# Kernel optimization log

Measured on AMD Instinct MI355X. Metric: run time of the kernel, lower is better.

The kernel has to match this reference:

```python
import jax, jax.numpy as jnp
import numpy as np

N = 50000
E = 800000
IN_C, HID_C, OUT_C = 5, 64, 32


def setup_inputs() -> dict:
    key = jax.random.key(0)
    ks = jax.random.split(key, 9)
    x = jax.random.normal(ks[0], (N, IN_C), dtype=jnp.float32)
    edge_index = jax.random.randint(ks[1], (2, E), 0, N, dtype=jnp.int64)
    # SAGEConv params: lin_l (neighbor path, has bias), lin_r (root path, no bias)
    def lin(k, fan_out, fan_in):
        s = 1.0 / np.sqrt(fan_in)
        return jax.random.uniform(k, (fan_out, fan_in), jnp.float32, -s, s)
    W1l = lin(ks[2], HID_C, IN_C); b1 = jnp.zeros((HID_C,), jnp.float32); W1r = lin(ks[3], HID_C, IN_C)
    W2l = lin(ks[4], HID_C, HID_C); b2 = jnp.zeros((HID_C,), jnp.float32); W2r = lin(ks[5], HID_C, HID_C)
    W3l = lin(ks[6], OUT_C, HID_C); b3 = jnp.zeros((OUT_C,), jnp.float32); W3r = lin(ks[7], OUT_C, HID_C)
    return {"x": x, "edge_index": edge_index,
            "W1l": W1l, "b1": b1, "W1r": W1r,
            "W2l": W2l, "b2": b2, "W2r": W2r,
            "W3l": W3l, "b3": b3, "W3r": W3r}


def _sage_conv(x, src, dst, inv_deg, Wl, bl, Wr):
    # PyG SAGEConv (aggr='mean'): out = lin_l(mean_j x_j) + lin_r(x)
    msg = x[src]                                          # [E, d_in] gather
    agg = jax.ops.segment_sum(msg, dst, num_segments=N)   # [N, d_in] scatter-add
    mean = agg * inv_deg                                  # mean aggregation
    return mean @ Wl.T + bl + x @ Wr.T


def reference(x, edge_index, W1l, b1, W1r, W2l, b2, W2r, W3l, b3, W3r):
    src, dst = edge_index[0], edge_index[1]
    deg = jax.ops.segment_sum(jnp.ones((E,), x.dtype), dst, num_segments=N)
    inv_deg = (1.0 / jnp.maximum(deg, 1.0))[:, None]      # [N, 1]
    h = jax.nn.relu(_sage_conv(x, src, dst, inv_deg, W1l, b1, W1r))
    # F.dropout(p=0.2, training=self.training): identity in eval mode
    h = jax.nn.relu(_sage_conv(h, src, dst, inv_deg, W2l, b2, W2r))
    out = _sage_conv(h, src, dst, inv_deg, W3l, b3, W3r)
    return out
```

## Files before the change

### kernel.cpp

```cpp
#include <hip/hip_runtime.h>
#include <hip/hip_fp16.h>


#define N_NODES 50000
#define N_EDGES 800000
#define IN_C 5
#define HID_C 64
#define OUT_C 32

#define NB 196
#define BCAP 6144
#define BWG 256
#define BCH (N_EDGES / BWG)

typedef __attribute__((ext_vector_type(8))) short bf16x8;
typedef __attribute__((ext_vector_type(4))) float f32x4;

__device__ __forceinline__ int rfl(int v) { return __builtin_amdgcn_readfirstlane(v); }
__device__ __forceinline__ float lanebc(float v, int l) {
    return __int_as_float(__builtin_amdgcn_readlane(__float_as_int(v), l));
}
__device__ __forceinline__ unsigned short f2bf(float f) {
    unsigned u = __float_as_uint(f);
    return (unsigned short)((u + 0x7fffu + ((u >> 16) & 1u)) >> 16);
}
__device__ __forceinline__ float bf2f(unsigned short b) {
    return __uint_as_float(((unsigned)b) << 16);
}
__device__ __forceinline__ float2 unpk_h2(unsigned u) {
    __half2 h = *(__half2*)&u;
    return __half22float2(h);
}


__global__ __launch_bounds__(256) void k_prep(
    const float* __restrict__ W2l, const float* __restrict__ W2r,
    const float* __restrict__ W3l, const float* __restrict__ W3r,
    unsigned short* __restrict__ W2hi, unsigned short* __restrict__ W2lo,
    unsigned short* __restrict__ W3hi, unsigned short* __restrict__ W3lo,
    int* __restrict__ gcur) {
    if (blockIdx.x == 0 && threadIdx.x < NB) gcur[threadIdx.x] = 0;
    const int t = blockIdx.x * 256 + threadIdx.x;
    const int stride = gridDim.x * 256;
    for (int p = t; p < 64 * 128; p += stride) {
        int j = p >> 7, k = p & 127;
        float w = (k < 64) ? W2l[j * 64 + k] : W2r[j * 64 + (k - 64)];
        unsigned short h = f2bf(w);
        W2hi[p] = h;
        W2lo[p] = f2bf(w - bf2f(h));
    }
    for (int p = t; p < 32 * 128; p += stride) {
        int j = p >> 7, k = p & 127;
        float w = (k < 64) ? W3l[j * 64 + k] : W3r[j * 64 + (k - 64)];
        unsigned short h = f2bf(w);
        W3hi[p] = h;
        W3lo[p] = f2bf(w - bf2f(h));
    }
}


__global__ __launch_bounds__(256) void k_bucket(const int* __restrict__ ei,
                                                int* __restrict__ gcur,
                                                unsigned* __restrict__ ebuf) {
    __shared__ int hist[NB];
    __shared__ int loff[NB];
    __shared__ int cur[NB];
    __shared__ int gbase[NB];
    __shared__ int scanb[256];
    __shared__ unsigned stage[BCH];
    const int t = threadIdx.x;
    const int c0 = blockIdx.x * BCH;

    if (t < NB) hist[t] = 0;
    __syncthreads();
    for (int i = t; i < BCH; i += 256) {
        int d = ei[N_EDGES + c0 + i];
        atomicAdd(&hist[d >> 8], 1);
    }
    __syncthreads();
    scanb[t] = (t < NB) ? hist[t] : 0;
    __syncthreads();
#pragma unroll
    for (int o = 1; o < 256; o <<= 1) {
        int v = scanb[t];
        int a = (t >= o) ? scanb[t - o] : 0;
        __syncthreads();
        scanb[t] = v + a;
        __syncthreads();
    }
    if (t < NB) {
        int ex = (t == 0) ? 0 : scanb[t - 1];
        loff[t] = ex;
        cur[t] = ex;
        gbase[t] = atomicAdd(&gcur[t], hist[t]);
    }
    __syncthreads();
    for (int i = t; i < BCH; i += 256) {
        int d = ei[N_EDGES + c0 + i];
        int s = ei[c0 + i];
        int b = d >> 8;
        int p = atomicAdd(&cur[b], 1);
        stage[p] = ((unsigned)d << 16) | (unsigned)s;
    }
    __syncthreads();
    for (int i = t; i < BCH; i += 256) {
        unsigned ev = stage[i];
        int b = ev >> 24;
        int pos = gbase[b] + (i - loff[b]);
        if (pos < BCAP) ebuf[b * BCAP + pos] = ev;
    }
}

__global__ __launch_bounds__(256) void k_bsort(const int* __restrict__ gcur,
                                               const unsigned* __restrict__ ebuf,
                                               int* __restrict__ row_off,
                                               float* __restrict__ inv_deg,
                                               int* __restrict__ srcs) {
    __shared__ int sc[256];
    __shared__ int cnt[256];
    __shared__ int loff[256];
    __shared__ int cur[256];
    __shared__ int stage[BCAP];
    const int t = threadIdx.x;
    const int b = blockIdx.x;

    sc[t] = (t < NB) ? gcur[t] : 0;
    __syncthreads();
#pragma unroll
    for (int o = 1; o < 256; o <<= 1) {
        int v = sc[t];
        int a = (t >= o) ? sc[t - o] : 0;
        __syncthreads();
        sc[t] = v + a;
        __syncthreads();
    }
    const int base = (b == 0) ? 0 : sc[b - 1];
    const int nraw = gcur[b];
    const int n = nraw < BCAP ? nraw : BCAP;
    const int node0 = b << 8;
    const unsigned* eb = ebuf + b * BCAP;

    cnt[t] = 0;
    __syncthreads();
    for (int i = t; i < n; i += 256) atomicAdd(&cnt[(eb[i] >> 16) & 255], 1);
    __syncthreads();
    loff[t] = cnt[t];
    __syncthreads();
#pragma unroll
    for (int o = 1; o < 256; o <<= 1) {
        int v = loff[t];
        int a = (t >= o) ? loff[t - o] : 0;
        __syncthreads();
        loff[t] = v + a;
        __syncthreads();
    }
    int ex = loff[t] - cnt[t];
    cur[t] = ex;
    int node = node0 + t;
    if (node < N_NODES) {
        row_off[node] = base + ex;
        int d = cnt[t];
        inv_deg[node] = 1.0f / (float)(d > 1 ? d : 1);
    }
    if (b == 0 && t == 0) row_off[N_NODES] = N_EDGES;
    __syncthreads();
    for (int i = t; i < n; i += 256) {
        unsigned ev = eb[i];
        int p = atomicAdd(&cur[(ev >> 16) & 255], 1);
        stage[p] = (int)(ev & 0xFFFFu);
    }
    __syncthreads();
    for (int i = t; i < n; i += 256) srcs[base + i] = stage[i];
}


__global__ __launch_bounds__(256) void k_layer1(
    const float* __restrict__ x, const int* __restrict__ row_off,
    const int* __restrict__ srcs, const float* __restrict__ inv_deg,
    const float* __restrict__ W1l, const float* __restrict__ b1,
    const float* __restrict__ W1r, __half* __restrict__ h1) {
    const int t = threadIdx.x;
    const int lane = t & 63;
    const int v = blockIdx.x * 4 + (t >> 6);
    if (v >= N_NODES) return;
    const int sub = lane >> 3;
    const int c = lane & 7;

    float wl[IN_C], wr[IN_C];
#pragma unroll
    for (int i = 0; i < IN_C; ++i) {
        wl[i] = W1l[lane * IN_C + i];
        wr[i] = W1r[lane * IN_C + i];
    }
    float bb = b1[lane];

    int beg = rfl(row_off[v]);
    int end = rfl(row_off[v + 1]);
    float sum = 0.f;
    for (int e = beg; e < end; e += 8) {
        int o = e + sub;
        if (o < end && c < IN_C) sum += x[srcs[o] * IN_C + c];
    }
    sum += __shfl_xor(sum, 8, 64);
    sum += __shfl_xor(sum, 16, 64);
    sum += __shfl_xor(sum, 32, 64);
    float summ = sum * inv_deg[v];
    float xv = (lane < IN_C) ? x[v * IN_C + lane] : 0.f;
    float acc = bb;
#pragma unroll
    for (int i = 0; i < IN_C; ++i) {
        acc += wl[i] * lanebc(summ, i);
        acc += wr[i] * lanebc(xv, i);
    }
    h1[v * HID_C + lane] = __float2half(fmaxf(acc, 0.f));
}


template <typename T> __device__ __forceinline__ T cvt_out(float v);
template <> __device__ __forceinline__ float cvt_out<float>(float v) { return v; }
template <> __device__ __forceinline__ __half cvt_out<__half>(float v) { return __float2half(v); }

template <int DOUT, bool RELU, typename OutT>
__global__ __launch_bounds__(256) void k_fused(
    const __half* __restrict__ h, const int* __restrict__ row_off,
    const int* __restrict__ srcs, const float* __restrict__ inv_deg,
    const unsigned short* __restrict__ Whi, const unsigned short* __restrict__ Wlo,
    const float* __restrict__ bias, OutT* __restrict__ out) {
    constexpr int AP = 152;
    __shared__ __align__(16) unsigned short Ah[32][AP];
    __shared__ __align__(16) unsigned short Al[32][AP];
    const int t = threadIdx.x;
    const int lane = t & 63;
    const int w = t >> 6;
    const int ns = lane >> 3;
    const int cg = lane & 7;
    const int node0 = blockIdx.x * 32;
    const int m = w * 8 + ns;
    const int v = node0 + m;
    const bool valid = v < N_NODES;
    const uint4* h4 = (const uint4*)h;

    int beg = 0, deg = 0;
    if (valid) {
        beg = row_off[v];
        deg = row_off[v + 1] - beg;
    }

    float s0 = 0.f, s1 = 0.f, s2 = 0.f, s3 = 0.f;
    float s4 = 0.f, s5 = 0.f, s6 = 0.f, s7 = 0.f;
    for (int k = 0; k < deg; k += 4) {
        int i0 = srcs[beg + k];
        int i1 = (k + 1 < deg) ? srcs[beg + k + 1] : i0;
        int i2 = (k + 2 < deg) ? srcs[beg + k + 2] : i0;
        int i3 = (k + 3 < deg) ? srcs[beg + k + 3] : i0;
        uint4 u0 = h4[i0 * 8 + cg];
        uint4 u1 = h4[i1 * 8 + cg];
        uint4 u2 = h4[i2 * 8 + cg];
        uint4 u3 = h4[i3 * 8 + cg];
        {
            float2 a = unpk_h2(u0.x), b = unpk_h2(u0.y);
            float2 c = unpk_h2(u0.z), d = unpk_h2(u0.w);
            s0 += a.x; s1 += a.y; s2 += b.x; s3 += b.y;
            s4 += c.x; s5 += c.y; s6 += d.x; s7 += d.y;
        }
        if (k + 1 < deg) {
            float2 a = unpk_h2(u1.x), b = unpk_h2(u1.y);
            float2 c = unpk_h2(u1.z), d = unpk_h2(u1.w);
            s0 += a.x; s1 += a.y; s2 += b.x; s3 += b.y;
            s4 += c.x; s5 += c.y; s6 += d.x; s7 += d.y;
        }
        if (k + 2 < deg) {
            float2 a = unpk_h2(u2.x), b = unpk_h2(u2.y);
            float2 c = unpk_h2(u2.z), d = unpk_h2(u2.w);
            s0 += a.x; s1 += a.y; s2 += b.x; s3 += b.y;
            s4 += c.x; s5 += c.y; s6 += d.x; s7 += d.y;
        }
        if (k + 3 < deg) {
            float2 a = unpk_h2(u3.x), b = unpk_h2(u3.y);
            float2 c = unpk_h2(u3.z), d = unpk_h2(u3.w);
            s0 += a.x; s1 += a.y; s2 += b.x; s3 += b.y;
            s4 += c.x; s5 += c.y; s6 += d.x; s7 += d.y;
        }
    }

    uint4 ur = make_uint4(0u, 0u, 0u, 0u);
    float idg = 0.f;
    if (valid) {
        ur = h4[v * 8 + cg];
        idg = inv_deg[v];
    }
    float m0 = s0 * idg, m1 = s1 * idg, m2 = s2 * idg, m3 = s3 * idg;
    float m4 = s4 * idg, m5 = s5 * idg, m6 = s6 * idg, m7 = s7 * idg;

    {
        unsigned short a0 = f2bf(m0), a1 = f2bf(m1), a2 = f2bf(m2), a3 = f2bf(m3);
        unsigned short a4 = f2bf(m4), a5 = f2bf(m5), a6 = f2bf(m6), a7 = f2bf(m7);
        uint4 hi, lo;
        hi.x = (unsigned)a0 | ((unsigned)a1 << 16);
        hi.y = (unsigned)a2 | ((unsigned)a3 << 16);
        hi.z = (unsigned)a4 | ((unsigned)a5 << 16);
        hi.w = (unsigned)a6 | ((unsigned)a7 << 16);
        lo.x = (unsigned)f2bf(m0 - bf2f(a0)) | ((unsigned)f2bf(m1 - bf2f(a1)) << 16);
        lo.y = (unsigned)f2bf(m2 - bf2f(a2)) | ((unsigned)f2bf(m3 - bf2f(a3)) << 16);
        lo.z = (unsigned)f2bf(m4 - bf2f(a4)) | ((unsigned)f2bf(m5 - bf2f(a5)) << 16);
        lo.w = (unsigned)f2bf(m6 - bf2f(a6)) | ((unsigned)f2bf(m7 - bf2f(a7)) << 16);
        *(uint4*)&Ah[m][cg * 8] = hi;
        *(uint4*)&Al[m][cg * 8] = lo;
    }
    {
        float2 p0 = unpk_h2(ur.x), p1 = unpk_h2(ur.y);
        float2 p2 = unpk_h2(ur.z), p3 = unpk_h2(ur.w);
        unsigned short a0 = f2bf(p0.x), a1 = f2bf(p0.y), a2 = f2bf(p1.x), a3 = f2bf(p1.y);
        unsigned short a4 = f2bf(p2.x), a5 = f2bf(p2.y), a6 = f2bf(p3.x), a7 = f2bf(p3.y);
        uint4 hi, lo;
        hi.x = (unsigned)a0 | ((unsigned)a1 << 16);
        hi.y = (unsigned)a2 | ((unsigned)a3 << 16);
        hi.z = (unsigned)a4 | ((unsigned)a5 << 16);
        hi.w = (unsigned)a6 | ((unsigned)a7 << 16);
        lo.x = (unsigned)f2bf(p0.x - bf2f(a0)) | ((unsigned)f2bf(p0.y - bf2f(a1)) << 16);
        lo.y = (unsigned)f2bf(p1.x - bf2f(a2)) | ((unsigned)f2bf(p1.y - bf2f(a3)) << 16);
        lo.z = (unsigned)f2bf(p2.x - bf2f(a4)) | ((unsigned)f2bf(p2.y - bf2f(a5)) << 16);
        lo.w = (unsigned)f2bf(p3.x - bf2f(a6)) | ((unsigned)f2bf(p3.y - bf2f(a7)) << 16);
        *(uint4*)&Ah[m][64 + cg * 8] = hi;
        *(uint4*)&Al[m][64 + cg * 8] = lo;
    }
    __syncthreads();

    constexpr int CT = DOUT / 16;
    constexpr int NTILES = 2 * CT;
    const int r = lane & 15;
    const int quad = lane >> 4;
#pragma unroll
    for (int ti = w; ti < NTILES; ti += 4) {
        const int n = ti % CT;
        const int rh = ti / CT;
        f32x4 acc = (f32x4){0.f, 0.f, 0.f, 0.f};
#pragma unroll
        for (int ks = 0; ks < 4; ++ks) {
            bf16x8 ah = *(const bf16x8*)&Ah[rh * 16 + r][ks * 32 + quad * 8];
            bf16x8 al = *(const bf16x8*)&Al[rh * 16 + r][ks * 32 + quad * 8];
            const size_t wb = ((size_t)(n * 16 + r)) * 128 + ks * 32 + quad * 8;
            bf16x8 bh = *(const bf16x8*)(Whi + wb);
            bf16x8 bl = *(const bf16x8*)(Wlo + wb);
            acc = __builtin_amdgcn_mfma_f32_16x16x32_bf16(ah, bh, acc, 0, 0, 0);
            acc = __builtin_amdgcn_mfma_f32_16x16x32_bf16(ah, bl, acc, 0, 0, 0);
            acc = __builtin_amdgcn_mfma_f32_16x16x32_bf16(al, bh, acc, 0, 0, 0);
        }
        float bv = bias[n * 16 + r];
#pragma unroll
        for (int g = 0; g < 4; ++g) {
            int node = node0 + rh * 16 + quad * 4 + g;
            if (node < N_NODES) {
                float vv = acc[g] + bv;
                if (RELU) vv = fmaxf(vv, 0.f);
                out[(size_t)node * DOUT + n * 16 + r] = cvt_out<OutT>(vv);
            }
        }
    }
}


extern "C" void kernel_launch(void* const* d_in, const int* in_sizes, int n_in,
                              void* d_out, int out_size, void* d_ws, size_t ws_size,
                              hipStream_t stream) {
    const float* x   = (const float*)d_in[0];
    const int*   ei  = (const int*)d_in[1];
    const float* W1l = (const float*)d_in[2];
    const float* b1  = (const float*)d_in[3];
    const float* W1r = (const float*)d_in[4];
    const float* W2l = (const float*)d_in[5];
    const float* b2  = (const float*)d_in[6];
    const float* W2r = (const float*)d_in[7];
    const float* W3l = (const float*)d_in[8];
    const float* b3  = (const float*)d_in[9];
    const float* W3r = (const float*)d_in[10];

    char* ws = (char*)d_ws;
    size_t off = 0;
    auto alloc = [&](size_t bytes) -> char* {
        char* p = ws + off;
        off += (bytes + 255) & ~(size_t)255;
        return p;
    };
    int*      gcur   = (int*)alloc(NB * sizeof(int));
    int*      rowoff = (int*)alloc((N_NODES + 1) * sizeof(int));
    float*    invdeg = (float*)alloc(N_NODES * sizeof(float));
    int*      srcs   = (int*)alloc(N_EDGES * sizeof(int));
    unsigned* ebuf   = (unsigned*)alloc((size_t)NB * BCAP * sizeof(unsigned));
    __half*   h1     = (__half*)alloc((size_t)N_NODES * HID_C * sizeof(__half));
    __half*   h2     = (__half*)alloc((size_t)N_NODES * HID_C * sizeof(__half));
    unsigned short* W2hi = (unsigned short*)alloc(64 * 128 * 2);
    unsigned short* W2lo = (unsigned short*)alloc(64 * 128 * 2);
    unsigned short* W3hi = (unsigned short*)alloc(32 * 128 * 2);
    unsigned short* W3lo = (unsigned short*)alloc(32 * 128 * 2);

    k_prep<<<dim3(48), dim3(256), 0, stream>>>(W2l, W2r, W3l, W3r,
                                               W2hi, W2lo, W3hi, W3lo, gcur);
    k_bucket<<<dim3(BWG), dim3(256), 0, stream>>>(ei, gcur, ebuf);
    k_bsort<<<dim3(NB), dim3(256), 0, stream>>>(gcur, ebuf, rowoff, invdeg, srcs);

    k_layer1<<<dim3(N_NODES / 4), dim3(256), 0, stream>>>(
        x, rowoff, srcs, invdeg, W1l, b1, W1r, h1);

    const int FT = (N_NODES + 31) / 32;
    k_fused<HID_C, true, __half><<<dim3(FT), dim3(256), 0, stream>>>(
        h1, rowoff, srcs, invdeg, W2hi, W2lo, b2, h2);

    k_fused<OUT_C, false, float><<<dim3(FT), dim3(256), 0, stream>>>(
        h2, rowoff, srcs, invdeg, W3hi, W3lo, b3, (float*)d_out);
}
```

Baseline: 170.5 us.

## Prefetch neighbor indices, cache edge words in LDS, and raise bucket block count

The bucketing kernel now runs with 800 workgroups instead of 256 and stages packed edge words in shared memory, so edge_index is read from global memory once instead of twice. The fused aggregation kernel software-pipelines neighbor index loads one iteration ahead and replaces the tail branches with weighted FMAs. It also hoists the root-feature and inverse-degree loads ahead of the gather loop, and layer 1 hoists its loads the same way. The aim is to hide index-load latency and cut redundant global traffic, at the cost of more LDS, extra registers and some wasted gathers on padded lanes.

```diff
diff --git a/kernel.cpp b/kernel.cpp
--- a/kernel.cpp
+++ b/kernel.cpp
@@ -10,7 +10,7 @@
 
 #define NB 196
 #define BCAP 6144
-#define BWG 256
+#define BWG 800
 #define BCH (N_EDGES / BWG)
 
 typedef __attribute__((ext_vector_type(8))) short bf16x8;
@@ -67,6 +67,7 @@
     __shared__ int cur[NB];
     __shared__ int gbase[NB];
     __shared__ int scanb[256];
+    __shared__ unsigned ev0[BCH];
     __shared__ unsigned stage[BCH];
     const int t = threadIdx.x;
     const int c0 = blockIdx.x * BCH;
@@ -74,7 +75,9 @@
     if (t < NB) hist[t] = 0;
     __syncthreads();
     for (int i = t; i < BCH; i += 256) {
+        int s = ei[c0 + i];
         int d = ei[N_EDGES + c0 + i];
+        ev0[i] = ((unsigned)d << 16) | (unsigned)s;
         atomicAdd(&hist[d >> 8], 1);
     }
     __syncthreads();
@@ -96,11 +99,10 @@
     }
     __syncthreads();
     for (int i = t; i < BCH; i += 256) {
-        int d = ei[N_EDGES + c0 + i];
-        int s = ei[c0 + i];
-        int b = d >> 8;
+        unsigned ev = ev0[i];
+        int b = ev >> 24;
         int p = atomicAdd(&cur[b], 1);
-        stage[p] = ((unsigned)d << 16) | (unsigned)s;
+        stage[p] = ev;
     }
     __syncthreads();
     for (int i = t; i < BCH; i += 256) {
@@ -196,6 +198,8 @@
 
     int beg = rfl(row_off[v]);
     int end = rfl(row_off[v + 1]);
+    float xv = (lane < IN_C) ? x[v * IN_C + lane] : 0.f;
+    float idg = inv_deg[v];
     float sum = 0.f;
     for (int e = beg; e < end; e += 8) {
         int o = e + sub;
@@ -204,8 +208,7 @@
     sum += __shfl_xor(sum, 8, 64);
     sum += __shfl_xor(sum, 16, 64);
     sum += __shfl_xor(sum, 32, 64);
-    float summ = sum * inv_deg[v];
-    float xv = (lane < IN_C) ? x[v * IN_C + lane] : 0.f;
+    float summ = sum * idg;
     float acc = bb;
 #pragma unroll
     for (int i = 0; i < IN_C; ++i) {
@@ -241,54 +244,64 @@
     const uint4* h4 = (const uint4*)h;
 
     int beg = 0, deg = 0;
+    float idg = 0.f;
+    uint4 ur = make_uint4(0u, 0u, 0u, 0u);
     if (valid) {
         beg = row_off[v];
         deg = row_off[v + 1] - beg;
-    }
+        idg = inv_deg[v];
+        ur = h4[v * 8 + cg];
+    }
+
+    const int* sp = srcs + beg;
+    const int last = (deg > 0) ? (deg - 1) : 0;
+#define SIDX(K) sp[(K) < last ? (K) : last]
+    int j0 = SIDX(0), j1 = SIDX(1), j2 = SIDX(2), j3 = SIDX(3);
 
     float s0 = 0.f, s1 = 0.f, s2 = 0.f, s3 = 0.f;
     float s4 = 0.f, s5 = 0.f, s6 = 0.f, s7 = 0.f;
     for (int k = 0; k < deg; k += 4) {
-        int i0 = srcs[beg + k];
-        int i1 = (k + 1 < deg) ? srcs[beg + k + 1] : i0;
-        int i2 = (k + 2 < deg) ? srcs[beg + k + 2] : i0;
-        int i3 = (k + 3 < deg) ? srcs[beg + k + 3] : i0;
-        uint4 u0 = h4[i0 * 8 + cg];
-        uint4 u1 = h4[i1 * 8 + cg];
-        uint4 u2 = h4[i2 * 8 + cg];
-        uint4 u3 = h4[i3 * 8 + cg];
+        uint4 u0 = h4[j0 * 8 + cg];
+        uint4 u1 = h4[j1 * 8 + cg];
+        uint4 u2 = h4[j2 * 8 + cg];
+        uint4 u3 = h4[j3 * 8 + cg];
+        float w1 = (k + 1 < deg) ? 1.f : 0.f;
+        float w2 = (k + 2 < deg) ? 1.f : 0.f;
+        float w3 = (k + 3 < deg) ? 1.f : 0.f;
+        j0 = SIDX(k + 4); j1 = SIDX(k + 5); j2 = SIDX(k + 6); j3 = SIDX(k + 7);
         {
             float2 a = unpk_h2(u0.x), b = unpk_h2(u0.y);
             float2 c = unpk_h2(u0.z), d = unpk_h2(u0.w);
             s0 += a.x; s1 += a.y; s2 += b.x; s3 += b.y;
             s4 += c.x; s5 += c.y; s6 += d.x; s7 += d.y;
         }
-        if (k + 1 < deg) {
+        {
             float2 a = unpk_h2(u1.x), b = unpk_h2(u1.y);
             float2 c = unpk_h2(u1.z), d = unpk_h2(u1.w);
-            s0 += a.x; s1 += a.y; s2 += b.x; s3 += b.y;
-            s4 += c.x; s5 += c.y; s6 += d.x; s7 += d.y;
-        }
-        if (k + 2 < deg) {
+            s0 = fmaf(a.x, w1, s0); s1 = fmaf(a.y, w1, s1);
+            s2 = fmaf(b.x, w1, s2); s3 = fmaf(b.y, w1, s3);
+            s4 = fmaf(c.x, w1, s4); s5 = fmaf(c.y, w1, s5);
+            s6 = fmaf(d.x, w1, s6); s7 = fmaf(d.y, w1, s7);
+        }
+        {
             float2 a = unpk_h2(u2.x), b = unpk_h2(u2.y);
             float2 c = unpk_h2(u2.z), d = unpk_h2(u2.w);
-            s0 += a.x; s1 += a.y; s2 += b.x; s3 += b.y;
-            s4 += c.x; s5 += c.y; s6 += d.x; s7 += d.y;
-        }
-        if (k + 3 < deg) {
+            s0 = fmaf(a.x, w2, s0); s1 = fmaf(a.y, w2, s1);
+            s2 = fmaf(b.x, w2, s2); s3 = fmaf(b.y, w2, s3);
+            s4 = fmaf(c.x, w2, s4); s5 = fmaf(c.y, w2, s5);
+            s6 = fmaf(d.x, w2, s6); s7 = fmaf(d.y, w2, s7);
+        }
+        {
             float2 a = unpk_h2(u3.x), b = unpk_h2(u3.y);
             float2 c = unpk_h2(u3.z), d = unpk_h2(u3.w);
-            s0 += a.x; s1 += a.y; s2 += b.x; s3 += b.y;
-            s4 += c.x; s5 += c.y; s6 += d.x; s7 += d.y;
-        }
-    }
-
-    uint4 ur = make_uint4(0u, 0u, 0u, 0u);
-    float idg = 0.f;
-    if (valid) {
-        ur = h4[v * 8 + cg];
-        idg = inv_deg[v];
-    }
+            s0 = fmaf(a.x, w3, s0); s1 = fmaf(a.y, w3, s1);
+            s2 = fmaf(b.x, w3, s2); s3 = fmaf(b.y, w3, s3);
+            s4 = fmaf(c.x, w3, s4); s5 = fmaf(c.y, w3, s5);
+            s6 = fmaf(d.x, w3, s6); s7 = fmaf(d.y, w3, s7);
+        }
+    }
+#undef SIDX
+
     float m0 = s0 * idg, m1 = s1 * idg, m2 = s2 * idg, m3 = s3 * idg;
     float m4 = s4 * idg, m5 = s5 * idg, m6 = s6 * idg, m7 = s7 * idg;
 
```

Result: slower. 174.7 us (+2.5%).
